# Kernel tuning notes

Hardware: AMD Instinct MI355X
Metric: run time of the kernel (lower is better)

Reference implementation:

```python
import jax, jax.numpy as jnp
import numpy as np

# Dimensions (must match init_kwargs)
IC = 8    # independent channels (one Linear each)
RC = 8    # regular channels
PC = 8    # parallel channels
G = 4     # shared-weight groups
IPG = 512 // G   # input length per group = 128
OPG = 512 // G   # output length per group = 128
B = 128


def setup_inputs() -> dict:
    key = jax.random.key(0)
    k1, k2, k3 = jax.random.split(key, 3)
    x = jax.random.normal(k1, (B, IC * RC, PC, IPG * G), dtype=jnp.float32)
    # Per-independent-channel Linear weights/biases (torch Linear: y = x @ W.T + b)
    bound = 1.0 / np.sqrt(IPG)
    W = jax.random.uniform(k2, (IC, OPG, IPG), dtype=jnp.float32, minval=-bound, maxval=bound)
    b = jax.random.uniform(k3, (IC, OPG), dtype=jnp.float32, minval=-bound, maxval=bound)
    return {"x": x, "W": W, "b": b}


def reference(x, W, b):
    Bx = x.shape[0]
    # view -> (B, IC, RC, PC, IPG*G); tensor_split along last + stack(dim=-2)
    # is a contiguous reshape -> (B, IC, RC, PC, G, IPG)
    xi = x.reshape(Bx, IC, RC, PC, G, IPG)
    # block-diagonal grouped GEMM: one Linear per independent channel i
    y = jnp.einsum('bicpgk,iok->bicpgo', xi, W) + b[None, :, None, None, None, :]
    # (B, IC, RC, PC, G, OPG) -> (B, IC*RC, PC, G*OPG)
    return y.reshape(Bx, IC * RC, PC, G * OPG)
```

## Files before the change

### kernel.cpp

```cpp
#include <hip/hip_runtime.h>
#include <hip/hip_bf16.h>

typedef __bf16 bf16x8 __attribute__((ext_vector_type(8)));
typedef __bf16 bf16x4 __attribute__((ext_vector_type(4)));
typedef float floatx4 __attribute__((ext_vector_type(4)));

#define IC 8
#define RC 8
#define PC 8
#define G_ 4
#define IPG 128
#define OPG 128

#define WROW 136

__global__ __launch_bounds__(256, 2)
void mcsl_kernel(const float* __restrict__ x,
                 const float* __restrict__ W,
                 const float* __restrict__ bias,
                 float* __restrict__ y)
{
    __shared__ __align__(16) __bf16 Wlds[128 * WROW];
    __shared__ float blds[128];

    const int blk = blockIdx.x;
    const int i = blk >> 8;
    const int blockRow = blk & 255;

    const float4* Wsrc = (const float4*)(W + (size_t)i * (OPG * IPG));
    for (int idx = threadIdx.x; idx < (OPG * IPG) / 4; idx += 256) {
        float4 w4 = Wsrc[idx];
        int o  = idx >> 5;
        int k4 = (idx & 31) << 2;
        bf16x4 wq;
        wq[0] = (__bf16)w4.x; wq[1] = (__bf16)w4.y;
        wq[2] = (__bf16)w4.z; wq[3] = (__bf16)w4.w;
        *(bf16x4*)&Wlds[o * WROW + k4] = wq;
    }
    if (threadIdx.x < 128) blds[threadIdx.x] = bias[i * OPG + threadIdx.x];
    __syncthreads();

    const int lane = threadIdx.x & 63;
    const int wv   = threadIdx.x >> 6;
    const int nrow = lane & 15;
    const int quad = lane >> 4;

    const int b_idx  = blockRow >> 1;
    const int r_base = (blockRow & 1) * 128;
    const float* xbase = x + ((size_t)(b_idx * IC + i) * (RC * PC * G_) + r_base) * IPG;
    float*       ybase = y + ((size_t)(b_idx * IC + i) * (RC * PC * G_) + r_base) * OPG;

    bf16x8 afrag[2][4];
    #pragma unroll
    for (int rt = 0; rt < 2; ++rt) {
        const float* rowp = xbase + (size_t)(wv * 32 + rt * 16 + nrow) * IPG;
        #pragma unroll
        for (int ks = 0; ks < 4; ++ks) {
            const float4* p = (const float4*)(rowp + ks * 32 + quad * 8);
            float4 a0 = p[0];
            float4 a1 = p[1];
            bf16x8 af;
            af[0] = (__bf16)a0.x; af[1] = (__bf16)a0.y;
            af[2] = (__bf16)a0.z; af[3] = (__bf16)a0.w;
            af[4] = (__bf16)a1.x; af[5] = (__bf16)a1.y;
            af[6] = (__bf16)a1.z; af[7] = (__bf16)a1.w;
            afrag[rt][ks] = af;
        }
    }

    floatx4 acc[2][8];
    #pragma unroll
    for (int rt = 0; rt < 2; ++rt)
        #pragma unroll
        for (int ct = 0; ct < 8; ++ct)
            acc[rt][ct] = (floatx4){0.f, 0.f, 0.f, 0.f};

    #pragma unroll
    for (int ks = 0; ks < 4; ++ks) {
        #pragma unroll
        for (int ct = 0; ct < 8; ++ct) {
            bf16x8 bfrag = *(const bf16x8*)&Wlds[(ct * 16 + nrow) * WROW + ks * 32 + quad * 8];
            acc[0][ct] = __builtin_amdgcn_mfma_f32_16x16x32_bf16(afrag[0][ks], bfrag, acc[0][ct], 0, 0, 0);
            acc[1][ct] = __builtin_amdgcn_mfma_f32_16x16x32_bf16(afrag[1][ks], bfrag, acc[1][ct], 0, 0, 0);
        }
    }

    #pragma unroll
    for (int rt = 0; rt < 2; ++rt) {
        const int rowl = wv * 32 + rt * 16 + quad * 4;
        #pragma unroll
        for (int ct = 0; ct < 8; ++ct) {
            float bo = blds[ct * 16 + nrow];
            #pragma unroll
            for (int r = 0; r < 4; ++r) {
                ybase[(size_t)(rowl + r) * OPG + ct * 16 + nrow] = acc[rt][ct][r] + bo;
            }
        }
    }
}

extern "C" void kernel_launch(void* const* d_in, const int* in_sizes, int n_in,
                              void* d_out, int out_size, void* d_ws, size_t ws_size,
                              hipStream_t stream) {
    const float* x = (const float*)d_in[0];
    const float* W = (const float*)d_in[1];
    const float* b = (const float*)d_in[2];
    float* y = (float*)d_out;
    dim3 grid(2048), block(256);
    hipLaunchKernelGGL(mcsl_kernel, grid, block, 0, stream, x, W, b, y);
}
```

Measured before the change: 267.3 us.

## Process 256 rows per block with register-prefetched LDS-staged x chunks

Each block now covers one (batch, channel) pair of 256 rows, handled as four 64-row chunks, and the grid is halved. The weight conversion into LDS is paid once per 256 rows instead of once per 128. The next chunk of x is prefetched into registers while MFMAs run on the current chunk staged in LDS. The x loads are now fully coalesced row-contiguous reads and occupancy is raised to 3 blocks per CU, at the cost of extra LDS, added barriers and fewer blocks in the grid.

```diff
diff --git a/kernel.cpp b/kernel.cpp
--- a/kernel.cpp
+++ b/kernel.cpp
@@ -13,22 +13,29 @@
 #define OPG 128
 
 #define WROW 136
+#define XROW 136
 
-__global__ __launch_bounds__(256, 2)
+__global__ __launch_bounds__(256, 3)
 void mcsl_kernel(const float* __restrict__ x,
                  const float* __restrict__ W,
                  const float* __restrict__ bias,
                  float* __restrict__ y)
 {
     __shared__ __align__(16) __bf16 Wlds[128 * WROW];
+    __shared__ __align__(16) __bf16 Xlds[64 * XROW];
     __shared__ float blds[128];
 
-    const int blk = blockIdx.x;
-    const int i = blk >> 8;
-    const int blockRow = blk & 255;
+    const int tid = threadIdx.x;
+    const int i = blockIdx.x & 7;
+    const int b = blockIdx.x >> 3;
+
+    const float* xbase = x + ((size_t)(b * (IC * RC) + i * RC)) * (PC * G_ * IPG);
+    float*       ybase = y + ((size_t)(b * (IC * RC) + i * RC)) * (PC * G_ * OPG);
 
     const float4* Wsrc = (const float4*)(W + (size_t)i * (OPG * IPG));
-    for (int idx = threadIdx.x; idx < (OPG * IPG) / 4; idx += 256) {
+    #pragma unroll
+    for (int it = 0; it < 16; ++it) {
+        int idx = tid + it * 256;
         float4 w4 = Wsrc[idx];
         int o  = idx >> 5;
         int k4 = (idx & 31) << 2;
@@ -37,64 +44,80 @@
         wq[2] = (__bf16)w4.z; wq[3] = (__bf16)w4.w;
         *(bf16x4*)&Wlds[o * WROW + k4] = wq;
     }
-    if (threadIdx.x < 128) blds[threadIdx.x] = bias[i * OPG + threadIdx.x];
+    if (tid < 128) blds[tid] = bias[i * OPG + tid];
+
+    float4 pf[8];
+    {
+        const float4* src = (const float4*)xbase;
+        #pragma unroll
+        for (int j = 0; j < 8; ++j) pf[j] = src[tid * 8 + j];
+    }
+    {
+        const int row = tid >> 2, col0 = (tid & 3) * 32;
+        #pragma unroll
+        for (int j = 0; j < 4; ++j) {
+            float4 a0 = pf[2 * j], a1 = pf[2 * j + 1];
+            bf16x8 v;
+            v[0] = (__bf16)a0.x; v[1] = (__bf16)a0.y; v[2] = (__bf16)a0.z; v[3] = (__bf16)a0.w;
+            v[4] = (__bf16)a1.x; v[5] = (__bf16)a1.y; v[6] = (__bf16)a1.z; v[7] = (__bf16)a1.w;
+            *(bf16x8*)&Xlds[row * XROW + col0 + j * 8] = v;
+        }
+    }
     __syncthreads();
 
-    const int lane = threadIdx.x & 63;
-    const int wv   = threadIdx.x >> 6;
+    const int lane = tid & 63;
+    const int wv   = tid >> 6;
     const int nrow = lane & 15;
     const int quad = lane >> 4;
 
-    const int b_idx  = blockRow >> 1;
-    const int r_base = (blockRow & 1) * 128;
-    const float* xbase = x + ((size_t)(b_idx * IC + i) * (RC * PC * G_) + r_base) * IPG;
-    float*       ybase = y + ((size_t)(b_idx * IC + i) * (RC * PC * G_) + r_base) * OPG;
+    #pragma unroll
+    for (int c = 0; c < 4; ++c) {
+        if (c < 3) {
+            const float4* src = (const float4*)(xbase + (size_t)(c + 1) * 64 * IPG);
+            #pragma unroll
+            for (int j = 0; j < 8; ++j) pf[j] = src[tid * 8 + j];
+        }
 
-    bf16x8 afrag[2][4];
-    #pragma unroll
-    for (int rt = 0; rt < 2; ++rt) {
-        const float* rowp = xbase + (size_t)(wv * 32 + rt * 16 + nrow) * IPG;
+        bf16x8 af[4];
+        #pragma unroll
+        for (int ks = 0; ks < 4; ++ks)
+            af[ks] = *(const bf16x8*)&Xlds[(wv * 16 + nrow) * XROW + ks * 32 + quad * 8];
+
+        floatx4 acc[8];
+        #pragma unroll
+        for (int ct = 0; ct < 8; ++ct) acc[ct] = (floatx4){0.f, 0.f, 0.f, 0.f};
+
         #pragma unroll
         for (int ks = 0; ks < 4; ++ks) {
-            const float4* p = (const float4*)(rowp + ks * 32 + quad * 8);
-            float4 a0 = p[0];
-            float4 a1 = p[1];
-            bf16x8 af;
-            af[0] = (__bf16)a0.x; af[1] = (__bf16)a0.y;
-            af[2] = (__bf16)a0.z; af[3] = (__bf16)a0.w;
-            af[4] = (__bf16)a1.x; af[5] = (__bf16)a1.y;
-            af[6] = (__bf16)a1.z; af[7] = (__bf16)a1.w;
-            afrag[rt][ks] = af;
+            #pragma unroll
+            for (int ct = 0; ct < 8; ++ct) {
+                bf16x8 bfrag = *(const bf16x8*)&Wlds[(ct * 16 + nrow) * WROW + ks * 32 + quad * 8];
+                acc[ct] = __builtin_amdgcn_mfma_f32_16x16x32_bf16(af[ks], bfrag, acc[ct], 0, 0, 0);
+            }
         }
-    }
 
-    floatx4 acc[2][8];
-    #pragma unroll
-    for (int rt = 0; rt < 2; ++rt)
-        #pragma unroll
-        for (int ct = 0; ct < 8; ++ct)
-            acc[rt][ct] = (floatx4){0.f, 0.f, 0.f, 0.f};
+        if (c < 3) {
+            __syncthreads();
+            const int row = tid >> 2, col0 = (tid & 3) * 32;
+            #pragma unroll
+            for (int j = 0; j < 4; ++j) {
+                float4 a0 = pf[2 * j], a1 = pf[2 * j + 1];
+                bf16x8 v;
+                v[0] = (__bf16)a0.x; v[1] = (__bf16)a0.y; v[2] = (__bf16)a0.z; v[3] = (__bf16)a0.w;
+                v[4] = (__bf16)a1.x; v[5] = (__bf16)a1.y; v[6] = (__bf16)a1.z; v[7] = (__bf16)a1.w;
+                *(bf16x8*)&Xlds[row * XROW + col0 + j * 8] = v;
+            }
+            __syncthreads();
+        }
 
-    #pragma unroll
-    for (int ks = 0; ks < 4; ++ks) {
-        #pragma unroll
-        for (int ct = 0; ct < 8; ++ct) {
-            bf16x8 bfrag = *(const bf16x8*)&Wlds[(ct * 16 + nrow) * WROW + ks * 32 + quad * 8];
-            acc[0][ct] = __builtin_amdgcn_mfma_f32_16x16x32_bf16(afrag[0][ks], bfrag, acc[0][ct], 0, 0, 0);
-            acc[1][ct] = __builtin_amdgcn_mfma_f32_16x16x32_bf16(afrag[1][ks], bfrag, acc[1][ct], 0, 0, 0);
-        }
-    }
-
-    #pragma unroll
-    for (int rt = 0; rt < 2; ++rt) {
-        const int rowl = wv * 32 + rt * 16 + quad * 4;
+        float* yc = ybase + (size_t)c * 64 * OPG;
+        const int rowl = wv * 16 + quad * 4;
         #pragma unroll
         for (int ct = 0; ct < 8; ++ct) {
             float bo = blds[ct * 16 + nrow];
             #pragma unroll
-            for (int r = 0; r < 4; ++r) {
-                ybase[(size_t)(rowl + r) * OPG + ct * 16 + nrow] = acc[rt][ct][r] + bo;
-            }
+            for (int r = 0; r < 4; ++r)
+                yc[(size_t)(rowl + r) * OPG + ct * 16 + nrow] = acc[ct][r] + bo;
         }
     }
 }
@@ -106,6 +129,6 @@
     const float* W = (const float*)d_in[1];
     const float* b = (const float*)d_in[2];
     float* y = (float*)d_out;
-    dim3 grid(2048), block(256);
+    dim3 grid(1024), block(256);
     hipLaunchKernelGGL(mcsl_kernel, grid, block, 0, stream, x, W, b, y);
 }
```

Result: faster. 247.7 us (-7.3%).

## Stage X tiles in LDS, keep W in registers, store outputs as float4

Applied to the files above, without the earlier changes.

The kernel now stages the 128x128 x tile in LDS as bf16 and keeps each wave's 32 output rows of W in registers, instead of loading W into LDS per block. The MFMA operands are swapped so each lane holds four consecutive output columns, which lets results go out as float4 stores rather than scalar strided stores. Block indexing is reordered so blocks sharing an i are spread out, and launch bounds are raised to 4 blocks per CU. The intent is to remove the per-block W conversion through LDS and the poorly coalesced scalar output writes, at the cost of an extra LDS round-trip for x and more register pressure.

```diff
diff --git a/kernel.cpp b/kernel.cpp
--- a/kernel.cpp
+++ b/kernel.cpp
@@ -5,97 +5,103 @@
 typedef __bf16 bf16x4 __attribute__((ext_vector_type(4)));
 typedef float floatx4 __attribute__((ext_vector_type(4)));
 
-#define IC 8
-#define RC 8
-#define PC 8
-#define G_ 4
-#define IPG 128
-#define OPG 128
+#define XROW 136
 
-#define WROW 136
+__global__ __launch_bounds__(256, 4)
+void mcsl_kernel(const float* __restrict__ x, const float* __restrict__ W,
+                 const float* __restrict__ bias, float* __restrict__ y)
+{
+    __shared__ __align__(16) __bf16 Xlds[128 * XROW];
 
-__global__ __launch_bounds__(256, 2)
-void mcsl_kernel(const float* __restrict__ x,
-                 const float* __restrict__ W,
-                 const float* __restrict__ bias,
-                 float* __restrict__ y)
-{
-    __shared__ __align__(16) __bf16 Wlds[128 * WROW];
-    __shared__ float blds[128];
+    const int tid  = threadIdx.x;
+    const int i    = blockIdx.x & 7;
+    const int b    = (blockIdx.x >> 3) & 127;
+    const int half = blockIdx.x >> 10;
 
-    const int blk = blockIdx.x;
-    const int i = blk >> 8;
-    const int blockRow = blk & 255;
+    const float* xb = x + (size_t)(b * 64 + i * 8) * 4096 + half * 16384;
+    float*       yb = y + (size_t)(b * 64 + i * 8) * 4096 + half * 16384;
 
-    const float4* Wsrc = (const float4*)(W + (size_t)i * (OPG * IPG));
-    for (int idx = threadIdx.x; idx < (OPG * IPG) / 4; idx += 256) {
-        float4 w4 = Wsrc[idx];
-        int o  = idx >> 5;
-        int k4 = (idx & 31) << 2;
-        bf16x4 wq;
-        wq[0] = (__bf16)w4.x; wq[1] = (__bf16)w4.y;
-        wq[2] = (__bf16)w4.z; wq[3] = (__bf16)w4.w;
-        *(bf16x4*)&Wlds[o * WROW + k4] = wq;
-    }
-    if (threadIdx.x < 128) blds[threadIdx.x] = bias[i * OPG + threadIdx.x];
-    __syncthreads();
-
-    const int lane = threadIdx.x & 63;
-    const int wv   = threadIdx.x >> 6;
+    const int lane = tid & 63;
+    const int wv   = tid >> 6;
     const int nrow = lane & 15;
     const int quad = lane >> 4;
 
-    const int b_idx  = blockRow >> 1;
-    const int r_base = (blockRow & 1) * 128;
-    const float* xbase = x + ((size_t)(b_idx * IC + i) * (RC * PC * G_) + r_base) * IPG;
-    float*       ybase = y + ((size_t)(b_idx * IC + i) * (RC * PC * G_) + r_base) * OPG;
+    const float4* xsrc = (const float4*)xb;
 
-    bf16x8 afrag[2][4];
+    float4 xf0[8];
     #pragma unroll
-    for (int rt = 0; rt < 2; ++rt) {
-        const float* rowp = xbase + (size_t)(wv * 32 + rt * 16 + nrow) * IPG;
+    for (int j = 0; j < 8; ++j) xf0[j] = xsrc[j * 256 + tid];
+
+    const float* wb = W + (size_t)i * 16384 + (wv * 32 + nrow) * 128 + quad * 8;
+    float4 wf[8][2];
+    #pragma unroll
+    for (int ot = 0; ot < 2; ++ot)
         #pragma unroll
         for (int ks = 0; ks < 4; ++ks) {
-            const float4* p = (const float4*)(rowp + ks * 32 + quad * 8);
-            float4 a0 = p[0];
-            float4 a1 = p[1];
-            bf16x8 af;
-            af[0] = (__bf16)a0.x; af[1] = (__bf16)a0.y;
-            af[2] = (__bf16)a0.z; af[3] = (__bf16)a0.w;
-            af[4] = (__bf16)a1.x; af[5] = (__bf16)a1.y;
-            af[6] = (__bf16)a1.z; af[7] = (__bf16)a1.w;
-            afrag[rt][ks] = af;
+            const float* p = wb + ot * 2048 + ks * 32;
+            wf[ot * 4 + ks][0] = *(const float4*)p;
+            wf[ot * 4 + ks][1] = *(const float4*)(p + 4);
         }
+
+    floatx4 bfrag[2];
+    #pragma unroll
+    for (int ot = 0; ot < 2; ++ot)
+        bfrag[ot] = *(const floatx4*)(bias + i * 128 + wv * 32 + ot * 16 + quad * 4);
+
+    #pragma unroll
+    for (int j = 0; j < 8; ++j) {
+        int idx = j * 256 + tid;
+        int row = idx >> 5, c4 = (idx & 31) * 4;
+        bf16x4 v;
+        v[0] = (__bf16)xf0[j].x; v[1] = (__bf16)xf0[j].y;
+        v[2] = (__bf16)xf0[j].z; v[3] = (__bf16)xf0[j].w;
+        *(bf16x4*)&Xlds[row * XROW + c4] = v;
     }
 
-    floatx4 acc[2][8];
+    float4 xf1[8];
     #pragma unroll
-    for (int rt = 0; rt < 2; ++rt)
-        #pragma unroll
-        for (int ct = 0; ct < 8; ++ct)
-            acc[rt][ct] = (floatx4){0.f, 0.f, 0.f, 0.f};
+    for (int j = 0; j < 8; ++j) xf1[j] = xsrc[(j + 8) * 256 + tid];
 
+    bf16x8 wfrag[8];
     #pragma unroll
-    for (int ks = 0; ks < 4; ++ks) {
-        #pragma unroll
-        for (int ct = 0; ct < 8; ++ct) {
-            bf16x8 bfrag = *(const bf16x8*)&Wlds[(ct * 16 + nrow) * WROW + ks * 32 + quad * 8];
-            acc[0][ct] = __builtin_amdgcn_mfma_f32_16x16x32_bf16(afrag[0][ks], bfrag, acc[0][ct], 0, 0, 0);
-            acc[1][ct] = __builtin_amdgcn_mfma_f32_16x16x32_bf16(afrag[1][ks], bfrag, acc[1][ct], 0, 0, 0);
-        }
+    for (int f = 0; f < 8; ++f) {
+        bf16x8 v;
+        v[0] = (__bf16)wf[f][0].x; v[1] = (__bf16)wf[f][0].y;
+        v[2] = (__bf16)wf[f][0].z; v[3] = (__bf16)wf[f][0].w;
+        v[4] = (__bf16)wf[f][1].x; v[5] = (__bf16)wf[f][1].y;
+        v[6] = (__bf16)wf[f][1].z; v[7] = (__bf16)wf[f][1].w;
+        wfrag[f] = v;
     }
 
     #pragma unroll
-    for (int rt = 0; rt < 2; ++rt) {
-        const int rowl = wv * 32 + rt * 16 + quad * 4;
+    for (int j = 0; j < 8; ++j) {
+        int idx = (j + 8) * 256 + tid;
+        int row = idx >> 5, c4 = (idx & 31) * 4;
+        bf16x4 v;
+        v[0] = (__bf16)xf1[j].x; v[1] = (__bf16)xf1[j].y;
+        v[2] = (__bf16)xf1[j].z; v[3] = (__bf16)xf1[j].w;
+        *(bf16x4*)&Xlds[row * XROW + c4] = v;
+    }
+    __syncthreads();
+
+    #pragma unroll
+    for (int rt = 0; rt < 8; ++rt) {
+        bf16x8 xfr[4];
         #pragma unroll
-        for (int ct = 0; ct < 8; ++ct) {
-            float bo = blds[ct * 16 + nrow];
-            #pragma unroll
-            for (int r = 0; r < 4; ++r) {
-                ybase[(size_t)(rowl + r) * OPG + ct * 16 + nrow] = acc[rt][ct][r] + bo;
-            }
+        for (int ks = 0; ks < 4; ++ks)
+            xfr[ks] = *(const bf16x8*)&Xlds[(rt * 16 + nrow) * XROW + ks * 32 + quad * 8];
+
+        floatx4 acc0 = {0.f, 0.f, 0.f, 0.f};
+        floatx4 acc1 = {0.f, 0.f, 0.f, 0.f};
+        #pragma unroll
+        for (int ks = 0; ks < 4; ++ks) {
+            acc0 = __builtin_amdgcn_mfma_f32_16x16x32_bf16(wfrag[ks],     xfr[ks], acc0, 0, 0, 0);
+            acc1 = __builtin_amdgcn_mfma_f32_16x16x32_bf16(wfrag[4 + ks], xfr[ks], acc1, 0, 0, 0);
         }
+
+        float* yrow = yb + (size_t)(rt * 16 + nrow) * 128 + wv * 32 + quad * 4;
+        *(floatx4*)yrow        = acc0 + bfrag[0];
+        *(floatx4*)(yrow + 16) = acc1 + bfrag[1];
     }
 }
 
```

Measured after the change: 247.7 us. 1.08x faster.
